# Optimization experiments

Measured on AMD Instinct MI355X. Metric: run time of the kernel, lower is better.

The kernel has to match this reference:

```python
import jax, jax.numpy as jnp
import numpy as np

EMBED_DIM = 1024
NUM_HEADS = 16
HEAD_DIM = EMBED_DIM // NUM_HEADS


def setup_inputs() -> dict:
    key = jax.random.key(0)
    kx, kw1, kb1, kw2, kb2 = jax.random.split(key, 5)
    B, T, C = 4, 2048, EMBED_DIM
    s = 1.0 / np.sqrt(C)
    return {
        "x": jax.random.normal(kx, (B, T, C), dtype=jnp.float32),
        "qkv_w": jax.random.uniform(kw1, (3 * C, C), jnp.float32, -s, s),
        "qkv_b": jax.random.uniform(kb1, (3 * C,), jnp.float32, -s, s),
        "out_w": jax.random.uniform(kw2, (C, C), jnp.float32, -s, s),
        "out_b": jax.random.uniform(kb2, (C,), jnp.float32, -s, s),
    }


def reference(x, qkv_w, qkv_b, out_w, out_b):
    B, T, C = x.shape
    H, D = NUM_HEADS, HEAD_DIM
    qkv = x @ qkv_w.T + qkv_b                      # [B,T,3C]
    qkv = qkv.reshape(B, T, 3, H, D)
    q = qkv[:, :, 0].transpose(0, 2, 1, 3)         # [B,H,T,D]
    k = qkv[:, :, 1].transpose(0, 2, 1, 3)
    v = qkv[:, :, 2].transpose(0, 2, 1, 3)
    att = jnp.einsum("bhqd,bhkd->bhqk", q, k) / jnp.sqrt(jnp.float32(D))
    causal = jnp.tril(jnp.ones((T, T), dtype=bool))
    att = jnp.where(causal, att, -jnp.inf)
    att = jax.nn.softmax(att, axis=-1)
    out = jnp.einsum("bhqk,bhkd->bhqd", att, v)    # [B,H,T,D]
    out = out.transpose(0, 2, 1, 3).reshape(B, T, C)
    return out @ out_w.T + out_b
```

## Files before the change

### kernel.cpp

```cpp
#include <hip/hip_runtime.h>
#include <stdint.h>

typedef _Float16 f16;
typedef _Float16 f16x2 __attribute__((ext_vector_type(2)));
typedef _Float16 f16x4 __attribute__((ext_vector_type(4)));
typedef _Float16 f16x8 __attribute__((ext_vector_type(8)));
typedef float f32x4 __attribute__((ext_vector_type(4)));
typedef float f32x16 __attribute__((ext_vector_type(16)));
typedef unsigned int u32;
typedef unsigned int u32x4 __attribute__((ext_vector_type(4)));
typedef int i32x2 __attribute__((ext_vector_type(2)));

#define LOG2E 1.44269504088896340736f

__device__ __forceinline__ f32x4 mfma_16x16x32(f16x8 a, f16x8 b, f32x4 c) {
    return __builtin_amdgcn_mfma_f32_16x16x32_f16(a, b, c, 0, 0, 0);
}
__device__ __forceinline__ f32x16 mfma_32x32x16(f16x8 a, f16x8 b, f32x16 c) {
    return __builtin_amdgcn_mfma_f32_32x32x16_f16(a, b, c, 0, 0, 0);
}

__device__ __forceinline__ void gload_lds16(const void* g, void* l) {
    __builtin_amdgcn_global_load_lds(
        (const __attribute__((address_space(1))) unsigned int*)g,
        (__attribute__((address_space(3))) unsigned int*)l, 16, 0, 0);
}

__device__ __forceinline__ f16x2 cvt_pk_f16(float a, float b) {
    return __builtin_bit_cast(f16x2, __builtin_amdgcn_cvt_pkrtz(a, b));
}

__device__ __forceinline__ void plswap_u32(u32& a, u32& b) {
    i32x2 r = __builtin_amdgcn_permlane32_swap((int)a, (int)b, false, false);
    a = (u32)r[0]; b = (u32)r[1];
}

__global__ void cast_f32_f16(const float* __restrict__ src, f16* __restrict__ dst, int n4) {
    int i = blockIdx.x * 256 + threadIdx.x;
    if (i >= n4) return;
    float4 v = reinterpret_cast<const float4*>(src)[i];
    f16x4 o;
    o[0] = (f16)v.x; o[1] = (f16)v.y; o[2] = (f16)v.z; o[3] = (f16)v.w;
    reinterpret_cast<f16x4*>(dst)[i] = o;
}

template<int MODE>
__global__ __launch_bounds__(256, 2)
void gemm_tn(const f16* __restrict__ A, const f16* __restrict__ W,
             const float* __restrict__ bias, void* __restrict__ outp,
             int M, int N, int K)
{
    __shared__ __align__(16) f16 As[2][128 * 32];
    __shared__ __align__(16) f16 Bs[2][128 * 32];

    const int lane = threadIdx.x & 63;
    const int wave = threadIdx.x >> 6;
    const int l15 = lane & 15, l4 = lane >> 4;

    const int nwg = (int)(gridDim.x * gridDim.y);
    int orig = (int)(blockIdx.y * gridDim.x + blockIdx.x);
    int cpx = nwg >> 3;
    int w = (orig & 7) * cpx + (orig >> 3);
    const int row0 = (w / (int)gridDim.x) * 128;
    const int col0 = (w % (int)gridDim.x) * 128;
    const int wr = wave >> 1, wc = wave & 1;

    f32x4 acc[4][4] = {};

    const int srow = lane >> 2;
    const int scol = (lane & 3) * 8;
    const int nk = K >> 5;

    #pragma unroll
    for (int it = 0; it < 2; ++it) {
        int chunk = it * 4 + wave;
        gload_lds16(A + (size_t)(row0 + chunk * 16 + srow) * K + scol, As[0] + chunk * 512);
        gload_lds16(W + (size_t)(col0 + chunk * 16 + srow) * K + scol, Bs[0] + chunk * 512);
    }
    __syncthreads();

    for (int i = 0; i < nk; ++i) {
        const int cur = i & 1;

        if (i + 1 < nk) {
            const int k1 = (i + 1) << 5;
            #pragma unroll
            for (int it = 0; it < 2; ++it) {
                int chunk = it * 4 + wave;
                gload_lds16(A + (size_t)(row0 + chunk * 16 + srow) * K + k1 + scol, As[cur ^ 1] + chunk * 512);
                gload_lds16(W + (size_t)(col0 + chunk * 16 + srow) * K + k1 + scol, Bs[cur ^ 1] + chunk * 512);
            }
        }

        f16x8 af[4], bf[4];
        #pragma unroll
        for (int m = 0; m < 4; ++m)
            af[m] = *reinterpret_cast<const f16x8*>(As[cur] + (wr * 64 + m * 16 + l15) * 32 + l4 * 8);
        #pragma unroll
        for (int n = 0; n < 4; ++n)
            bf[n] = *reinterpret_cast<const f16x8*>(Bs[cur] + (wc * 64 + n * 16 + l15) * 32 + l4 * 8);
        #pragma unroll
        for (int m = 0; m < 4; ++m)
            #pragma unroll
            for (int n = 0; n < 4; ++n)
                acc[m][n] = mfma_16x16x32(af[m], bf[n], acc[m][n]);

        __syncthreads();
    }

    if (MODE == 0) {
        f16* qb = (f16*)outp;
        const size_t HS = (size_t)64 * 2048 * 64;
        #pragma unroll
        for (int m = 0; m < 4; ++m) {
            int rbase = row0 + wr * 64 + m * 16 + l4 * 4;
            #pragma unroll
            for (int n = 0; n < 4; ++n) {
                int j = col0 + wc * 64 + n * 16 + l15;
                int which = j >> 10;
                int h = (j >> 6) & 15;
                int d = j & 63;
                float bj = bias[j];
                f16* base = qb + (size_t)which * HS;
                float scale = (which == 0) ? (0.125f * LOG2E) : 1.0f;
                #pragma unroll
                for (int r = 0; r < 4; ++r) {
                    int row = rbase + r;
                    int b = row >> 11, t = row & 2047;
                    size_t off = ((size_t)(b * 16 + h) * 2048 + t) * 64 + d;
                    base[off] = (f16)((acc[m][n][r] + bj) * scale);
                }
            }
        }
    } else {
        float* O = (float*)outp;
        #pragma unroll
        for (int m = 0; m < 4; ++m) {
            int rbase = row0 + wr * 64 + m * 16 + l4 * 4;
            #pragma unroll
            for (int n = 0; n < 4; ++n) {
                int j = col0 + wc * 64 + n * 16 + l15;
                float bj = bias[j];
                #pragma unroll
                for (int r = 0; r < 4; ++r)
                    O[(size_t)(rbase + r) * N + j] = acc[m][n][r] + bj;
            }
        }
    }
}

__global__ __launch_bounds__(256, 4)
void attn_kernel(const f16* __restrict__ qb, const f16* __restrict__ kb,
                 const f16* __restrict__ vb, f16* __restrict__ ob)
{
    __shared__ __align__(16) f16 Ks[2][4096];
    __shared__ __align__(16) f16 Vs[2][64][68];

    const int tid = (int)threadIdx.x;
    const int bh = (int)blockIdx.x;
    const int qblk = (int)gridDim.y - 1 - (int)blockIdx.y;
    const int lane = tid & 63;
    const int wave = tid >> 6;
    const int l31 = lane & 31;
    const int hi  = lane >> 5;
    const int q0 = qblk * 128;
    const int qw = q0 + wave * 32;

    const f16* Qp = qb + ((size_t)bh * 2048 + qw) * 64;
    f16x8 qf[4];
    #pragma unroll
    for (int ss = 0; ss < 4; ++ss)
        qf[ss] = *reinterpret_cast<const f16x8*>(Qp + l31 * 64 + ss * 16 + hi * 8);

    float Mr = -1e30f, Lr = 0.0f;
    f32x16 oacc[2] = {};

    const int ntiles = 2 * qblk + 2;
    const f16* Kbh = kb + (size_t)bh * 2048 * 64;
    const f16* Vbh = vb + (size_t)bh * 2048 * 64;

    f16x8 vld0, vld1;
    {
        #pragma unroll
        for (int it = 0; it < 2; ++it) {
            int c = it * 4 + wave;
            gload_lds16(Kbh + lane * 64 + c * 8, &Ks[0][0] + c * 512);
        }
        vld0 = *reinterpret_cast<const f16x8*>(Vbh + lane * 64 + (wave * 2 + 0) * 8);
        vld1 = *reinterpret_cast<const f16x8*>(Vbh + lane * 64 + (wave * 2 + 1) * 8);
    }

    for (int t = 0; t < ntiles; ++t) {
        const int cur = t & 1;
        const int kv0 = t * 64;

        #pragma unroll
        for (int it = 0; it < 2; ++it) {
            int dblk = wave * 2 + it;
            const f16x8 v = it ? vld1 : vld0;
            #pragma unroll
            for (int e = 0; e < 8; ++e)
                Vs[cur][dblk * 8 + e][lane] = v[e];
        }

        __syncthreads();

        {
            const int kvn = (t + 1 < ntiles) ? (t + 1) * 64 : t * 64;
            const f16* Ktn = Kbh + (size_t)kvn * 64;
            #pragma unroll
            for (int it = 0; it < 2; ++it) {
                int c = it * 4 + wave;
                gload_lds16(Ktn + lane * 64 + c * 8, &Ks[cur ^ 1][0] + c * 512);
            }
            const f16* Vtn = Vbh + (size_t)kvn * 64;
            vld0 = *reinterpret_cast<const f16x8*>(Vtn + lane * 64 + (wave * 2 + 0) * 8);
            vld1 = *reinterpret_cast<const f16x8*>(Vtn + lane * 64 + (wave * 2 + 1) * 8);
        }

        if (kv0 <= qw + 31) {
            const f16* Ksc = &Ks[cur][0];

            f32x16 s0 = {}, s1 = {};
            __builtin_amdgcn_s_setprio(1);
            #pragma unroll
            for (int ss = 0; ss < 4; ++ss) {
                f16x8 kf0 = *reinterpret_cast<const f16x8*>(Ksc + (2 * ss + hi) * 512 + l31 * 8);
                f16x8 kf1 = *reinterpret_cast<const f16x8*>(Ksc + (2 * ss + hi) * 512 + (32 + l31) * 8);
                s0 = mfma_32x32x16(kf0, qf[ss], s0);
                s1 = mfma_32x32x16(kf1, qf[ss], s1);
            }
            __builtin_amdgcn_s_setprio(0);

            if (kv0 + 63 > qw) {
                const int qg = qw + l31;
                #pragma unroll
                for (int r = 0; r < 16; ++r) {
                    int k0g = kv0 + (r & 3) + 8 * (r >> 2) + 4 * hi;
                    if (k0g > qg)      s0[r] = -1e30f;
                    if (k0g + 32 > qg) s1[r] = -1e30f;
                }
            }

            float t16[16];
            #pragma unroll
            for (int i = 0; i < 16; ++i) t16[i] = fmaxf(s0[i], s1[i]);
            #pragma unroll
            for (int st = 8; st > 0; st >>= 1)
                #pragma unroll
                for (int i = 0; i < st; ++i) t16[i] = fmaxf(t16[i], t16[i + st]);
            float mx = t16[0];
            mx = fmaxf(mx, __shfl_xor(mx, 32));

            if (__any(mx > Mr + 8.0f)) {
                float nm = fmaxf(Mr, mx);
                float alpha = exp2f(Mr - nm);
                Mr = nm; Lr *= alpha;
                float ar[16];
                #pragma unroll
                for (int r = 0; r < 16; ++r)
                    ar[r] = __shfl(alpha, (r & 3) + 8 * (r >> 2) + 4 * hi);
                #pragma unroll
                for (int r = 0; r < 16; ++r) { oacc[0][r] *= ar[r]; oacc[1][r] *= ar[r]; }
            }

            float e0[16], e1[16];
            #pragma unroll
            for (int r = 0; r < 16; ++r) {
                e0[r] = exp2f(s0[r] - Mr);
                e1[r] = exp2f(s1[r] - Mr);
            }
            float sm[16];
            #pragma unroll
            for (int i = 0; i < 16; ++i) sm[i] = e0[i] + e1[i];
            #pragma unroll
            for (int st = 8; st > 0; st >>= 1)
                #pragma unroll
                for (int i = 0; i < st; ++i) sm[i] += sm[i + st];
            float rs = sm[0];
            rs += __shfl_xor(rs, 32);
            Lr += rs;

            u32 cpk[2][8];
            #pragma unroll
            for (int B = 0; B < 4; ++B) {
                cpk[0][2 * B]     = __builtin_bit_cast(u32, __builtin_amdgcn_cvt_pkrtz(e0[4 * B],     e0[4 * B + 1]));
                cpk[0][2 * B + 1] = __builtin_bit_cast(u32, __builtin_amdgcn_cvt_pkrtz(e0[4 * B + 2], e0[4 * B + 3]));
                cpk[1][2 * B]     = __builtin_bit_cast(u32, __builtin_amdgcn_cvt_pkrtz(e1[4 * B],     e1[4 * B + 1]));
                cpk[1][2 * B + 1] = __builtin_bit_cast(u32, __builtin_amdgcn_cvt_pkrtz(e1[4 * B + 2], e1[4 * B + 3]));
            }

            __builtin_amdgcn_s_setprio(1);
            #pragma unroll
            for (int ss = 0; ss < 4; ++ss) {
                const int kbi = ss >> 1, qq = ss & 1;
                u32 a0 = cpk[kbi][4 * qq + 0], b0 = cpk[kbi][4 * qq + 2];
                u32 a1 = cpk[kbi][4 * qq + 1], b1 = cpk[kbi][4 * qq + 3];
                plswap_u32(a0, b0);
                plswap_u32(a1, b1);
                u32x4 up; up[0] = a0; up[1] = a1; up[2] = b0; up[3] = b1;
                f16x8 pa = __builtin_bit_cast(f16x8, up);
                #pragma unroll
                for (int db = 0; db < 2; ++db) {
                    const f16* vp = &Vs[cur][db * 32 + l31][16 * ss + 8 * hi];
                    f16x4 v0 = *reinterpret_cast<const f16x4*>(vp);
                    f16x4 v1 = *reinterpret_cast<const f16x4*>(vp + 4);
                    f16x8 vf = __builtin_shufflevector(v0, v1, 0, 1, 2, 3, 4, 5, 6, 7);
                    oacc[db] = mfma_32x32x16(pa, vf, oacc[db]);
                }
            }
            __builtin_amdgcn_s_setprio(0);
        }
    }

    float rcp = 1.0f / Lr;
    float rr[16];
    #pragma unroll
    for (int r = 0; r < 16; ++r)
        rr[r] = __shfl(rcp, (r & 3) + 8 * (r >> 2) + 4 * hi);

    const int b = bh >> 4, h = bh & 15;
    f16* O = ob + ((size_t)b * 2048 + qw) * 1024 + h * 64;
    #pragma unroll
    for (int db = 0; db < 2; ++db)
        #pragma unroll
        for (int r = 0; r < 16; ++r) {
            int q = (r & 3) + 8 * (r >> 2) + 4 * hi;
            O[(size_t)q * 1024 + db * 32 + l31] = (f16)(oacc[db][r] * rr[r]);
        }
}

extern "C" void kernel_launch(void* const* d_in, const int* in_sizes, int n_in,
                              void* d_out, int out_size, void* d_ws, size_t ws_size,
                              hipStream_t stream)
{
    const float* x    = (const float*)d_in[0];
    const float* qkvw = (const float*)d_in[1];
    const float* qkvb = (const float*)d_in[2];
    const float* outw = (const float*)d_in[3];
    const float* outb = (const float*)d_in[4];
    float* out = (float*)d_out;

    f16* x_h    = (f16*)d_ws;
    f16* qkvw_h = x_h + (size_t)8192 * 1024;
    f16* outw_h = qkvw_h + (size_t)3072 * 1024;
    f16* q_buf  = outw_h + (size_t)1024 * 1024;
    f16* att_o  = q_buf + (size_t)3 * 8388608;

    cast_f32_f16<<<8192, 256, 0, stream>>>(x, x_h, 2097152);
    cast_f32_f16<<<3072, 256, 0, stream>>>(qkvw, qkvw_h, 786432);
    cast_f32_f16<<<1024, 256, 0, stream>>>(outw, outw_h, 262144);

    gemm_tn<0><<<dim3(24, 64), 256, 0, stream>>>(x_h, qkvw_h, qkvb, q_buf, 8192, 3072, 1024);
    attn_kernel<<<dim3(64, 16), 256, 0, stream>>>(q_buf, q_buf + 8388608, q_buf + 2 * 8388608, att_o);
    gemm_tn<1><<<dim3(8, 64), 256, 0, stream>>>(att_o, outw_h, outb, out, 8192, 1024, 1024);
}
```

Baseline: 195.3 us.

## Split long causal attention rows across two blocks and single-buffer GEMM LDS

The attention kernel now splits the eight longest query blocks into two KV halves, each handled by its own workgroup. Each half stores a partial output with its max and sum, and a new combine kernel merges them by log-sum-exp weighting. The aim is to even out the causal load imbalance, where the longest blocks dominate the tail. Separately, the GEMM drops its LDS double buffering in favour of a single buffer with two barriers per K step. That halves shared memory but exposes global load latency, and the extra kernel launch and partial-result traffic add overhead.

```diff
diff --git a/kernel.cpp b/kernel.cpp
--- a/kernel.cpp
+++ b/kernel.cpp
@@ -26,10 +26,6 @@
         (__attribute__((address_space(3))) unsigned int*)l, 16, 0, 0);
 }
 
-__device__ __forceinline__ f16x2 cvt_pk_f16(float a, float b) {
-    return __builtin_bit_cast(f16x2, __builtin_amdgcn_cvt_pkrtz(a, b));
-}
-
 __device__ __forceinline__ void plswap_u32(u32& a, u32& b) {
     i32x2 r = __builtin_amdgcn_permlane32_swap((int)a, (int)b, false, false);
     a = (u32)r[0]; b = (u32)r[1];
@@ -50,8 +46,8 @@
              const float* __restrict__ bias, void* __restrict__ outp,
              int M, int N, int K)
 {
-    __shared__ __align__(16) f16 As[2][128 * 32];
-    __shared__ __align__(16) f16 Bs[2][128 * 32];
+    __shared__ __align__(16) f16 As[128 * 32];
+    __shared__ __align__(16) f16 Bs[128 * 32];
 
     const int lane = threadIdx.x & 63;
     const int wave = threadIdx.x >> 6;
@@ -69,43 +65,31 @@
 
     const int srow = lane >> 2;
     const int scol = (lane & 3) * 8;
-    const int nk = K >> 5;
-
-    #pragma unroll
-    for (int it = 0; it < 2; ++it) {
-        int chunk = it * 4 + wave;
-        gload_lds16(A + (size_t)(row0 + chunk * 16 + srow) * K + scol, As[0] + chunk * 512);
-        gload_lds16(W + (size_t)(col0 + chunk * 16 + srow) * K + scol, Bs[0] + chunk * 512);
-    }
-    __syncthreads();
-
-    for (int i = 0; i < nk; ++i) {
-        const int cur = i & 1;
-
-        if (i + 1 < nk) {
-            const int k1 = (i + 1) << 5;
-            #pragma unroll
-            for (int it = 0; it < 2; ++it) {
-                int chunk = it * 4 + wave;
-                gload_lds16(A + (size_t)(row0 + chunk * 16 + srow) * K + k1 + scol, As[cur ^ 1] + chunk * 512);
-                gload_lds16(W + (size_t)(col0 + chunk * 16 + srow) * K + k1 + scol, Bs[cur ^ 1] + chunk * 512);
-            }
-        }
+
+    for (int k0 = 0; k0 < K; k0 += 32) {
+        __syncthreads();
+        #pragma unroll
+        for (int it = 0; it < 2; ++it) {
+            int chunk = it * 4 + wave;
+            const f16* gA = A + (size_t)(row0 + chunk * 16 + srow) * K + k0 + scol;
+            gload_lds16(gA, As + chunk * 512);
+            const f16* gB = W + (size_t)(col0 + chunk * 16 + srow) * K + k0 + scol;
+            gload_lds16(gB, Bs + chunk * 512);
+        }
+        __syncthreads();
 
         f16x8 af[4], bf[4];
         #pragma unroll
         for (int m = 0; m < 4; ++m)
-            af[m] = *reinterpret_cast<const f16x8*>(As[cur] + (wr * 64 + m * 16 + l15) * 32 + l4 * 8);
+            af[m] = *reinterpret_cast<const f16x8*>(As + (wr * 64 + m * 16 + l15) * 32 + l4 * 8);
         #pragma unroll
         for (int n = 0; n < 4; ++n)
-            bf[n] = *reinterpret_cast<const f16x8*>(Bs[cur] + (wc * 64 + n * 16 + l15) * 32 + l4 * 8);
+            bf[n] = *reinterpret_cast<const f16x8*>(Bs + (wc * 64 + n * 16 + l15) * 32 + l4 * 8);
         #pragma unroll
         for (int m = 0; m < 4; ++m)
             #pragma unroll
             for (int n = 0; n < 4; ++n)
                 acc[m][n] = mfma_16x16x32(af[m], bf[n], acc[m][n]);
-
-        __syncthreads();
     }
 
     if (MODE == 0) {
@@ -151,18 +135,31 @@
 
 __global__ __launch_bounds__(256, 4)
 void attn_kernel(const f16* __restrict__ qb, const f16* __restrict__ kb,
-                 const f16* __restrict__ vb, f16* __restrict__ ob)
+                 const f16* __restrict__ vb, f16* __restrict__ ob,
+                 f16* __restrict__ o0buf, float* __restrict__ Ms, float* __restrict__ Ls)
 {
     __shared__ __align__(16) f16 Ks[2][4096];
     __shared__ __align__(16) f16 Vs[2][64][68];
 
     const int tid = (int)threadIdx.x;
     const int bh = (int)blockIdx.x;
-    const int qblk = (int)gridDim.y - 1 - (int)blockIdx.y;
+    const int y = (int)blockIdx.y;
     const int lane = tid & 63;
     const int wave = tid >> 6;
     const int l31 = lane & 31;
     const int hi  = lane >> 5;
+
+    int qblk, t0, t1, mode;
+    if (y < 16) {
+        qblk = 15 - (y >> 1);
+        const int hn = qblk + 1;
+        if ((y & 1) == 0) { t0 = 0;  t1 = hn;     mode = 1; }
+        else              { t0 = hn; t1 = 2 * hn; mode = 2; }
+    } else {
+        qblk = 23 - y;
+        t0 = 0; t1 = 2 * qblk + 2; mode = 0;
+    }
+
     const int q0 = qblk * 128;
     const int qw = q0 + wave * 32;
 
@@ -175,23 +172,24 @@
     float Mr = -1e30f, Lr = 0.0f;
     f32x16 oacc[2] = {};
 
-    const int ntiles = 2 * qblk + 2;
     const f16* Kbh = kb + (size_t)bh * 2048 * 64;
     const f16* Vbh = vb + (size_t)bh * 2048 * 64;
 
     f16x8 vld0, vld1;
     {
+        const f16* Kt = Kbh + (size_t)t0 * 64 * 64;
         #pragma unroll
         for (int it = 0; it < 2; ++it) {
             int c = it * 4 + wave;
-            gload_lds16(Kbh + lane * 64 + c * 8, &Ks[0][0] + c * 512);
-        }
-        vld0 = *reinterpret_cast<const f16x8*>(Vbh + lane * 64 + (wave * 2 + 0) * 8);
-        vld1 = *reinterpret_cast<const f16x8*>(Vbh + lane * 64 + (wave * 2 + 1) * 8);
-    }
-
-    for (int t = 0; t < ntiles; ++t) {
-        const int cur = t & 1;
+            gload_lds16(Kt + lane * 64 + c * 8, &Ks[0][0] + c * 512);
+        }
+        const f16* Vt = Vbh + (size_t)t0 * 64 * 64;
+        vld0 = *reinterpret_cast<const f16x8*>(Vt + lane * 64 + (wave * 2 + 0) * 8);
+        vld1 = *reinterpret_cast<const f16x8*>(Vt + lane * 64 + (wave * 2 + 1) * 8);
+    }
+
+    for (int t = t0; t < t1; ++t) {
+        const int cur = (t - t0) & 1;
         const int kv0 = t * 64;
 
         #pragma unroll
@@ -206,7 +204,7 @@
         __syncthreads();
 
         {
-            const int kvn = (t + 1 < ntiles) ? (t + 1) * 64 : t * 64;
+            const int kvn = (t + 1 < t1) ? (t + 1) * 64 : t * 64;
             const f16* Ktn = Kbh + (size_t)kvn * 64;
             #pragma unroll
             for (int it = 0; it < 2; ++it) {
@@ -319,15 +317,59 @@
     for (int r = 0; r < 16; ++r)
         rr[r] = __shfl(rcp, (r & 3) + 8 * (r >> 2) + 4 * hi);
 
-    const int b = bh >> 4, h = bh & 15;
-    f16* O = ob + ((size_t)b * 2048 + qw) * 1024 + h * 64;
+    if (mode == 1) {
+        f16* O = o0buf + ((size_t)bh * 1024 + (qw - 1024)) * 64;
+        #pragma unroll
+        for (int db = 0; db < 2; ++db)
+            #pragma unroll
+            for (int r = 0; r < 16; ++r) {
+                int q = (r & 3) + 8 * (r >> 2) + 4 * hi;
+                O[(size_t)q * 64 + db * 32 + l31] = (f16)(oacc[db][r] * rr[r]);
+            }
+    } else {
+        const int b = bh >> 4, h = bh & 15;
+        f16* O = ob + ((size_t)b * 2048 + qw) * 1024 + h * 64;
+        #pragma unroll
+        for (int db = 0; db < 2; ++db)
+            #pragma unroll
+            for (int r = 0; r < 16; ++r) {
+                int q = (r & 3) + 8 * (r >> 2) + 4 * hi;
+                O[(size_t)q * 1024 + db * 32 + l31] = (f16)(oacc[db][r] * rr[r]);
+            }
+    }
+    if (mode != 0 && hi == 0) {
+        int si = (mode - 1) * 65536 + bh * 1024 + (qw - 1024) + l31;
+        Ms[si] = Mr;
+        Ls[si] = Lr;
+    }
+}
+
+__global__ void attn_combine(const f16* __restrict__ o0buf, const float* __restrict__ Ms,
+                             const float* __restrict__ Ls, f16* __restrict__ ob)
+{
+    int idx = blockIdx.x * 256 + threadIdx.x;
+    int d8 = idx & 7;
+    int q  = (idx >> 3) & 1023;
+    int bh = idx >> 13;
+    int b = bh >> 4, h = bh & 15;
+    int si = bh * 1024 + q;
+
+    float m0 = Ms[si], m1 = Ms[65536 + si];
+    float l0 = Ls[si], l1 = Ls[65536 + si];
+    float m = fmaxf(m0, m1);
+    float w0 = l0 * exp2f(m0 - m);
+    float w1 = l1 * exp2f(m1 - m);
+    float inv = 1.0f / (w0 + w1);
+    w0 *= inv; w1 *= inv;
+
+    f16x8 a = *reinterpret_cast<const f16x8*>(o0buf + (size_t)si * 64 + d8 * 8);
+    f16* po = ob + ((size_t)b * 2048 + 1024 + q) * 1024 + h * 64 + d8 * 8;
+    f16x8 c = *reinterpret_cast<const f16x8*>(po);
+    f16x8 o;
     #pragma unroll
-    for (int db = 0; db < 2; ++db)
-        #pragma unroll
-        for (int r = 0; r < 16; ++r) {
-            int q = (r & 3) + 8 * (r >> 2) + 4 * hi;
-            O[(size_t)q * 1024 + db * 32 + l31] = (f16)(oacc[db][r] * rr[r]);
-        }
+    for (int e = 0; e < 8; ++e)
+        o[e] = (f16)(w0 * (float)a[e] + w1 * (float)c[e]);
+    *reinterpret_cast<f16x8*>(po) = o;
 }
 
 extern "C" void kernel_launch(void* const* d_in, const int* in_sizes, int n_in,
@@ -346,12 +388,17 @@
     f16* outw_h = qkvw_h + (size_t)3072 * 1024;
     f16* q_buf  = outw_h + (size_t)1024 * 1024;
     f16* att_o  = q_buf + (size_t)3 * 8388608;
+    f16* o0buf  = att_o + (size_t)8192 * 1024;
+    float* Ms   = (float*)(o0buf + (size_t)64 * 1024 * 64);
+    float* Ls   = Ms + 2 * 65536;
 
     cast_f32_f16<<<8192, 256, 0, stream>>>(x, x_h, 2097152);
     cast_f32_f16<<<3072, 256, 0, stream>>>(qkvw, qkvw_h, 786432);
     cast_f32_f16<<<1024, 256, 0, stream>>>(outw, outw_h, 262144);
 
     gemm_tn<0><<<dim3(24, 64), 256, 0, stream>>>(x_h, qkvw_h, qkvb, q_buf, 8192, 3072, 1024);
-    attn_kernel<<<dim3(64, 16), 256, 0, stream>>>(q_buf, q_buf + 8388608, q_buf + 2 * 8388608, att_o);
+    attn_kernel<<<dim3(64, 24), 256, 0, stream>>>(q_buf, q_buf + 8388608, q_buf + 2 * 8388608,
+                                                  att_o, o0buf, Ms, Ls);
+    attn_combine<<<2048, 256, 0, stream>>>(o0buf, Ms, Ls, att_o);
     gemm_tn<1><<<dim3(8, 64), 256, 0, stream>>>(att_o, outw_h, outb, out, 8192, 1024, 1024);
 }
```

After: 210.0 us. +7.6%, slower.
